# Kernel tuning notes

Hardware: AMD Instinct MI355X
Metric: run time of the kernel (lower is better)

## Reference

```python
import jax, jax.numpy as jnp
import numpy as np

HEAD_NUM = 16

def setup_inputs() -> dict:
    key = jax.random.key(0)
    kq, kk, kv = jax.random.split(key, 3)
    shape = (4, 2048, 1024)  # [B, N, C]
    return {
        "query_layer": jax.random.normal(kq, shape, dtype=jnp.float32),
        "key_layer": jax.random.normal(kk, shape, dtype=jnp.float32),
        "value_layer": jax.random.normal(kv, shape, dtype=jnp.float32),
    }

def _split_heads(x, h):
    B, N, C = x.shape
    return x.reshape(B, N, h, C // h).transpose(0, 2, 1, 3)  # [B,H,N,d]

def reference(query_layer, key_layer, value_layer):
    B, N, C = query_layer.shape
    h = HEAD_NUM
    d = C // h
    q = _split_heads(query_layer, h)
    k = _split_heads(key_layer, h)
    v = _split_heads(value_layer, h)
    scores = jnp.einsum('bhnd,bhmd->bhnm', q, k) / jnp.sqrt(jnp.asarray(d, q.dtype))
    probs = jax.nn.softmax(scores, axis=-1)
    ctx = jnp.einsum('bhnm,bhmd->bhnd', probs, v)
    return ctx.transpose(0, 2, 1, 3).reshape(B, N, C)
```

## Files before the change

kernel.cpp:

```cpp
#include <hip/hip_runtime.h>
#include <hip/hip_bf16.h>

#define B_   4
#define N_   2048
#define C_   1024
#define NT   32
#define QSCALE 0.18033688011112042f

typedef __attribute__((ext_vector_type(8)))  short short8;
typedef __attribute__((ext_vector_type(4)))  float f32x4;
typedef __attribute__((ext_vector_type(16))) float f32x16;
typedef __attribute__((ext_vector_type(2)))  int   int2v;

__device__ __forceinline__ unsigned short f2bf(float x) {
    union { __hip_bfloat16 h; unsigned short u; } c;
    c.h = __float2bfloat16(x);
    return c.u;
}
__device__ __forceinline__ float fast_exp2(float x) {
    float r; asm("v_exp_f32 %0, %1" : "=v"(r) : "v"(x)); return r;
}
__device__ __forceinline__ int cvtpk(float a, float b) {
    int r; asm("v_cvt_pk_bf16_f32 %0, %1, %2" : "=v"(r) : "v"(a), "v"(b)); return r;
}

__global__ __launch_bounds__(256) void prepack(
    const float* __restrict__ K, const float* __restrict__ V,
    unsigned short* __restrict__ Kt, unsigned short* __restrict__ Vt)
{
    __shared__ __align__(16) unsigned short vl[64 * 64];
    const int blk = blockIdx.x;
    const int t = blk & 31, head = blk >> 5;
    const int b = head >> 4, h = head & 15;
    const int tid = threadIdx.x;
    const int r = tid >> 2, cb = tid & 3;
    const size_t head_off = (size_t)b * N_ * C_ + (size_t)h * 64;
    const int kv0 = t * 64;

    {
        const float* src = K + head_off + (size_t)(kv0 + r) * C_ + cb * 16;
        f32x4 x0 = *(const f32x4*)(src);
        f32x4 x1 = *(const f32x4*)(src + 4);
        f32x4 x2 = *(const f32x4*)(src + 8);
        f32x4 x3 = *(const f32x4*)(src + 12);
        short8 p0, p1;
        #pragma unroll
        for (int i = 0; i < 4; ++i) {
            p0[i] = (short)f2bf(x0[i]); p0[i + 4] = (short)f2bf(x1[i]);
            p1[i] = (short)f2bf(x2[i]); p1[i + 4] = (short)f2bf(x3[i]);
        }
        unsigned short* dst = Kt + (size_t)blk * 4096 + r * 64;
        const int swz = (r & 7) << 3;
        *(short8*)&dst[(cb * 16) ^ swz]     = p0;
        *(short8*)&dst[(cb * 16 + 8) ^ swz] = p1;
    }
    {
        const float* src = V + head_off + (size_t)(kv0 + r) * C_ + cb * 16;
        f32x4 y0 = *(const f32x4*)(src);
        f32x4 y1 = *(const f32x4*)(src + 4);
        f32x4 y2 = *(const f32x4*)(src + 8);
        f32x4 y3 = *(const f32x4*)(src + 12);
        #pragma unroll
        for (int i = 0; i < 4; ++i) {
            vl[(cb * 16 + i) * 64 + r]      = f2bf(y0[i]);
            vl[(cb * 16 + 4 + i) * 64 + r]  = f2bf(y1[i]);
            vl[(cb * 16 + 8 + i) * 64 + r]  = f2bf(y2[i]);
            vl[(cb * 16 + 12 + i) * 64 + r] = f2bf(y3[i]);
        }
    }
    __syncthreads();
    {
        short8 q0 = *(const short8*)&vl[r * 64 + cb * 16];
        short8 q1 = *(const short8*)&vl[r * 64 + cb * 16 + 8];
        unsigned short* dst = Vt + (size_t)blk * 4096 + r * 64;
        const int swz = (r & 7) << 3;
        *(short8*)&dst[(cb * 16) ^ swz]     = q0;
        *(short8*)&dst[(cb * 16 + 8) ^ swz] = q1;
    }
}

__global__ __launch_bounds__(256, 4) void attn_fwd(
    const float* __restrict__ Q, const unsigned short* __restrict__ Kt,
    const unsigned short* __restrict__ Vt, float* __restrict__ O)
{
    __shared__ __align__(16) unsigned short klds[2][4096];
    __shared__ __align__(16) unsigned short vlds[2][4096];

    const int L = blockIdx.x;
    const int xcd = L & 7;
    const int j = L >> 3;
    const int head = xcd + 8 * (j >> 4);
    const int qt = j & 15;
    const int b = head >> 4, h = head & 15;

    const int tid  = threadIdx.x;
    const int wave = tid >> 6;
    const int lane = tid & 63;
    const int l31  = lane & 31;
    const int hi   = lane >> 5;
    const int sw8  = (l31 & 7) << 3;

    const unsigned short* kbase = Kt + (size_t)head * (NT * 4096);
    const unsigned short* vbase = Vt + (size_t)head * (NT * 4096);
    const float* qp = Q + (size_t)b * N_ * C_ + (size_t)h * 64;
    float*       op = O + (size_t)b * N_ * C_ + (size_t)h * 64;

    const int qrow = qt * 128 + wave * 32 + l31;
    short8 qfrag[4];
    {
        const float* qr = qp + (size_t)qrow * C_ + hi * 8;
        #pragma unroll
        for (int ks = 0; ks < 4; ++ks) {
            f32x4 x0 = *(const f32x4*)(qr + ks * 16);
            f32x4 x1 = *(const f32x4*)(qr + ks * 16 + 4);
            short8 a;
            #pragma unroll
            for (int i = 0; i < 4; ++i) {
                a[i]     = (short)f2bf(x0[i] * QSCALE);
                a[i + 4] = (short)f2bf(x1[i] * QSCALE);
            }
            qfrag[ks] = a;
        }
    }

    f32x16 o0 = {}, o1 = {};
    float m_r = -3.0e38f, l_r = 0.0f;

    auto stage = [&](int t, int buf) {
        const unsigned short* kg = kbase + (size_t)t * 4096 + wave * 512 + lane * 8;
        const unsigned short* vg = vbase + (size_t)t * 4096 + wave * 512 + lane * 8;
        __builtin_amdgcn_global_load_lds((const __attribute__((address_space(1))) void*)kg,
            (__attribute__((address_space(3))) void*)&klds[buf][wave * 512], 16, 0, 0);
        __builtin_amdgcn_global_load_lds((const __attribute__((address_space(1))) void*)(kg + 2048),
            (__attribute__((address_space(3))) void*)&klds[buf][2048 + wave * 512], 16, 0, 0);
        __builtin_amdgcn_global_load_lds((const __attribute__((address_space(1))) void*)vg,
            (__attribute__((address_space(3))) void*)&vlds[buf][wave * 512], 16, 0, 0);
        __builtin_amdgcn_global_load_lds((const __attribute__((address_space(1))) void*)(vg + 2048),
            (__attribute__((address_space(3))) void*)&vlds[buf][2048 + wave * 512], 16, 0, 0);
    };

    stage(0, 0);
    int cur = 0;

    for (int t = 0; t < NT; ++t) {
        asm volatile("s_waitcnt vmcnt(0)" ::: "memory");
        __syncthreads();
        if (t + 1 < NT) stage(t + 1, cur ^ 1);

        const unsigned short* kl = klds[cur];
        const unsigned short* vl = vlds[cur];

        f32x16 s0 = {}, s1 = {};
        __builtin_amdgcn_s_setprio(1);
        #pragma unroll
        for (int ks = 0; ks < 4; ++ks) {
            const int cofs = (ks * 16 + hi * 8) ^ sw8;
            short8 kf0 = *(const short8*)&kl[l31 * 64 + cofs];
            short8 kf1 = *(const short8*)&kl[(32 + l31) * 64 + cofs];
            s0 = __builtin_amdgcn_mfma_f32_32x32x16_bf16(kf0, qfrag[ks], s0, 0, 0, 0);
            s1 = __builtin_amdgcn_mfma_f32_32x32x16_bf16(kf1, qfrag[ks], s1, 0, 0, 0);
        }
        __builtin_amdgcn_s_setprio(0);

        float mx[16];
        #pragma unroll
        for (int r = 0; r < 16; ++r) mx[r] = fmaxf(s0[r], s1[r]);
        #pragma unroll
        for (int st = 8; st; st >>= 1) {
            #pragma unroll
            for (int r = 0; r < st; ++r) mx[r] = fmaxf(mx[r], mx[r + st]);
        }
        int2v msw = __builtin_amdgcn_permlane32_swap(__float_as_int(mx[0]), __float_as_int(mx[0]), false, false);
        const float rm = fmaxf(__int_as_float(msw[0]), __int_as_float(msw[1]));

        if (!__all(rm - m_r <= 8.0f)) {
            const float mnew = fmaxf(m_r, rm);
            const float corr = fast_exp2(m_r - mnew);
            m_r = mnew;
            l_r *= corr;
            #pragma unroll
            for (int r = 0; r < 16; ++r) { o0[r] *= corr; o1[r] *= corr; }
        }

        #pragma unroll
        for (int r = 0; r < 16; ++r) {
            s0[r] = fast_exp2(s0[r] - m_r);
            s1[r] = fast_exp2(s1[r] - m_r);
        }
        float aa[16];
        #pragma unroll
        for (int r = 0; r < 16; ++r) aa[r] = s0[r] + s1[r];
        #pragma unroll
        for (int st = 8; st; st >>= 1) {
            #pragma unroll
            for (int r = 0; r < st; ++r) aa[r] += aa[r + st];
        }
        int2v ssw = __builtin_amdgcn_permlane32_swap(__float_as_int(aa[0]), __float_as_int(aa[0]), false, false);
        l_r += __int_as_float(ssw[0]) + __int_as_float(ssw[1]);

        short8 pf[4];
        #pragma unroll
        for (int ct = 0; ct < 2; ++ct) {
            #pragma unroll
            for (int kss = 0; kss < 2; ++kss) {
                float e0, e1, e2, e3, e4, e5, e6, e7;
                if (ct == 0) {
                    e0 = s0[8*kss+0]; e1 = s0[8*kss+1]; e2 = s0[8*kss+2]; e3 = s0[8*kss+3];
                    e4 = s0[8*kss+4]; e5 = s0[8*kss+5]; e6 = s0[8*kss+6]; e7 = s0[8*kss+7];
                } else {
                    e0 = s1[8*kss+0]; e1 = s1[8*kss+1]; e2 = s1[8*kss+2]; e3 = s1[8*kss+3];
                    e4 = s1[8*kss+4]; e5 = s1[8*kss+5]; e6 = s1[8*kss+6]; e7 = s1[8*kss+7];
                }
                int w0 = cvtpk(e0, e1);
                int w1 = cvtpk(e2, e3);
                int w2 = cvtpk(e4, e5);
                int w3 = cvtpk(e6, e7);
                int2v sA = __builtin_amdgcn_permlane32_swap(w0, w2, false, false);
                int2v sB = __builtin_amdgcn_permlane32_swap(w1, w3, false, false);
                union { int i[4]; short8 v; } u;
                u.i[0] = sA[0]; u.i[1] = sB[0]; u.i[2] = sA[1]; u.i[3] = sB[1];
                pf[ct * 2 + kss] = u.v;
            }
        }

        __builtin_amdgcn_s_setprio(1);
        #pragma unroll
        for (int ks = 0; ks < 4; ++ks) {
            const int cofs = (ks * 16 + hi * 8) ^ sw8;
            short8 vf0 = *(const short8*)&vl[l31 * 64 + cofs];
            short8 vf1 = *(const short8*)&vl[(32 + l31) * 64 + cofs];
            o0 = __builtin_amdgcn_mfma_f32_32x32x16_bf16(vf0, pf[ks], o0, 0, 0, 0);
            o1 = __builtin_amdgcn_mfma_f32_32x32x16_bf16(vf1, pf[ks], o1, 0, 0, 0);
        }
        __builtin_amdgcn_s_setprio(0);

        cur ^= 1;
    }

    const float inv = 1.0f / l_r;
    float* orow = op + (size_t)qrow * C_;
    #pragma unroll
    for (int bb = 0; bb < 4; ++bb) {
        f32x4 w0, w1;
        #pragma unroll
        for (int i = 0; i < 4; ++i) {
            w0[i] = o0[4 * bb + i] * inv;
            w1[i] = o1[4 * bb + i] * inv;
        }
        *(f32x4*)(orow + 8 * bb + 4 * hi)      = w0;
        *(f32x4*)(orow + 32 + 8 * bb + 4 * hi) = w1;
    }
}

extern "C" void kernel_launch(void* const* d_in, const int* in_sizes, int n_in,
                              void* d_out, int out_size, void* d_ws, size_t ws_size,
                              hipStream_t stream) {
    const float* q = (const float*)d_in[0];
    const float* k = (const float*)d_in[1];
    const float* v = (const float*)d_in[2];
    float* o = (float*)d_out;
    unsigned short* Kt = (unsigned short*)d_ws;
    unsigned short* Vt = Kt + (size_t)64 * NT * 4096;
    prepack<<<dim3(64 * NT), dim3(256), 0, stream>>>(k, v, Kt, Vt);
    attn_fwd<<<dim3(1024), dim3(256), 0, stream>>>(q, Kt, Vt, o);
}
```

Before: 115.0 us.

## Prepack K/V in MFMA fragment order and load fragments directly from global

The prepack kernel now writes K and V tiles in the exact per-lane MFMA fragment order, staging through swizzled LDS, and its blocks are mapped so each XCD handles particular heads. The attention kernel drops its LDS double buffer, barriers and vmcnt waits, and loads each fragment straight from global memory with contiguous 16-byte per-lane reads, relying on the L2 cache for reuse across the 16 query tiles of a head. The max and sum reductions are also restructured to use fewer serial steps. The risk is that global-load latency is no longer hidden by async staging and that L2 and bandwidth pressure rises, since each wave now fetches the K/V tiles itself instead of sharing one copy through LDS.

```diff
diff --git a/kernel.cpp b/kernel.cpp
--- a/kernel.cpp
+++ b/kernel.cpp
@@ -28,14 +28,19 @@
     const float* __restrict__ K, const float* __restrict__ V,
     unsigned short* __restrict__ Kt, unsigned short* __restrict__ Vt)
 {
-    __shared__ __align__(16) unsigned short vl[64 * 64];
-    const int blk = blockIdx.x;
-    const int t = blk & 31, head = blk >> 5;
+    __shared__ __align__(16) unsigned short kl[4096];
+    __shared__ __align__(16) unsigned short vl[4096];
+    const int L = blockIdx.x;
+    const int xcd = L & 7;
+    const int j = L >> 3;
+    const int head = xcd + 8 * (j >> 5);
+    const int t = j & 31;
     const int b = head >> 4, h = head & 15;
     const int tid = threadIdx.x;
     const int r = tid >> 2, cb = tid & 3;
     const size_t head_off = (size_t)b * N_ * C_ + (size_t)h * 64;
     const int kv0 = t * 64;
+    const int blk_out = head * NT + t;
 
     {
         const float* src = K + head_off + (size_t)(kv0 + r) * C_ + cb * 16;
@@ -49,10 +54,9 @@
             p0[i] = (short)f2bf(x0[i]); p0[i + 4] = (short)f2bf(x1[i]);
             p1[i] = (short)f2bf(x2[i]); p1[i + 4] = (short)f2bf(x3[i]);
         }
-        unsigned short* dst = Kt + (size_t)blk * 4096 + r * 64;
         const int swz = (r & 7) << 3;
-        *(short8*)&dst[(cb * 16) ^ swz]     = p0;
-        *(short8*)&dst[(cb * 16 + 8) ^ swz] = p1;
+        *(short8*)&kl[r * 64 + ((cb * 16) ^ swz)]     = p0;
+        *(short8*)&kl[r * 64 + ((cb * 16 + 8) ^ swz)] = p1;
     }
     {
         const float* src = V + head_off + (size_t)(kv0 + r) * C_ + cb * 16;
@@ -62,20 +66,29 @@
         f32x4 y3 = *(const f32x4*)(src + 12);
         #pragma unroll
         for (int i = 0; i < 4; ++i) {
-            vl[(cb * 16 + i) * 64 + r]      = f2bf(y0[i]);
-            vl[(cb * 16 + 4 + i) * 64 + r]  = f2bf(y1[i]);
-            vl[(cb * 16 + 8 + i) * 64 + r]  = f2bf(y2[i]);
-            vl[(cb * 16 + 12 + i) * 64 + r] = f2bf(y3[i]);
+            int d0 = cb * 16 + i;
+            vl[d0 * 64 + (r ^ ((d0 & 7) << 3))] = f2bf(y0[i]);
+            int d1 = cb * 16 + 4 + i;
+            vl[d1 * 64 + (r ^ ((d1 & 7) << 3))] = f2bf(y1[i]);
+            int d2 = cb * 16 + 8 + i;
+            vl[d2 * 64 + (r ^ ((d2 & 7) << 3))] = f2bf(y2[i]);
+            int d3 = cb * 16 + 12 + i;
+            vl[d3 * 64 + (r ^ ((d3 & 7) << 3))] = f2bf(y3[i]);
         }
     }
     __syncthreads();
-    {
-        short8 q0 = *(const short8*)&vl[r * 64 + cb * 16];
-        short8 q1 = *(const short8*)&vl[r * 64 + cb * 16 + 8];
-        unsigned short* dst = Vt + (size_t)blk * 4096 + r * 64;
-        const int swz = (r & 7) << 3;
-        *(short8*)&dst[(cb * 16) ^ swz]     = q0;
-        *(short8*)&dst[(cb * 16 + 8) ^ swz] = q1;
+    #pragma unroll
+    for (int cc = 0; cc < 2; ++cc) {
+        const int c  = tid + cc * 256;
+        const int f  = c >> 6;
+        const int ln = c & 63;
+        const int row = (f & 1) * 32 + (ln & 31);
+        const int col = (f >> 1) * 16 + (ln >> 5) * 8;
+        const int sw  = (row & 7) << 3;
+        short8 kk = *(const short8*)&kl[row * 64 + (col ^ sw)];
+        short8 vv = *(const short8*)&vl[row * 64 + (col ^ sw)];
+        *(short8*)&Kt[(size_t)blk_out * 4096 + c * 8] = kk;
+        *(short8*)&Vt[(size_t)blk_out * 4096 + c * 8] = vv;
     }
 }
 
@@ -83,9 +96,6 @@
     const float* __restrict__ Q, const unsigned short* __restrict__ Kt,
     const unsigned short* __restrict__ Vt, float* __restrict__ O)
 {
-    __shared__ __align__(16) unsigned short klds[2][4096];
-    __shared__ __align__(16) unsigned short vlds[2][4096];
-
     const int L = blockIdx.x;
     const int xcd = L & 7;
     const int j = L >> 3;
@@ -98,7 +108,6 @@
     const int lane = tid & 63;
     const int l31  = lane & 31;
     const int hi   = lane >> 5;
-    const int sw8  = (l31 & 7) << 3;
 
     const unsigned short* kbase = Kt + (size_t)head * (NT * 4096);
     const unsigned short* vbase = Vt + (size_t)head * (NT * 4096);
@@ -126,47 +135,28 @@
     f32x16 o0 = {}, o1 = {};
     float m_r = -3.0e38f, l_r = 0.0f;
 
-    auto stage = [&](int t, int buf) {
-        const unsigned short* kg = kbase + (size_t)t * 4096 + wave * 512 + lane * 8;
-        const unsigned short* vg = vbase + (size_t)t * 4096 + wave * 512 + lane * 8;
-        __builtin_amdgcn_global_load_lds((const __attribute__((address_space(1))) void*)kg,
-            (__attribute__((address_space(3))) void*)&klds[buf][wave * 512], 16, 0, 0);
-        __builtin_amdgcn_global_load_lds((const __attribute__((address_space(1))) void*)(kg + 2048),
-            (__attribute__((address_space(3))) void*)&klds[buf][2048 + wave * 512], 16, 0, 0);
-        __builtin_amdgcn_global_load_lds((const __attribute__((address_space(1))) void*)vg,
-            (__attribute__((address_space(3))) void*)&vlds[buf][wave * 512], 16, 0, 0);
-        __builtin_amdgcn_global_load_lds((const __attribute__((address_space(1))) void*)(vg + 2048),
-            (__attribute__((address_space(3))) void*)&vlds[buf][2048 + wave * 512], 16, 0, 0);
-    };
-
-    stage(0, 0);
-    int cur = 0;
+    const int lofs = lane * 8;
 
     for (int t = 0; t < NT; ++t) {
-        asm volatile("s_waitcnt vmcnt(0)" ::: "memory");
-        __syncthreads();
-        if (t + 1 < NT) stage(t + 1, cur ^ 1);
-
-        const unsigned short* kl = klds[cur];
-        const unsigned short* vl = vlds[cur];
+        const unsigned short* ktp = kbase + (size_t)t * 4096;
+        const unsigned short* vtp = vbase + (size_t)t * 4096;
 
         f32x16 s0 = {}, s1 = {};
         __builtin_amdgcn_s_setprio(1);
         #pragma unroll
         for (int ks = 0; ks < 4; ++ks) {
-            const int cofs = (ks * 16 + hi * 8) ^ sw8;
-            short8 kf0 = *(const short8*)&kl[l31 * 64 + cofs];
-            short8 kf1 = *(const short8*)&kl[(32 + l31) * 64 + cofs];
+            short8 kf0 = *(const short8*)(ktp + ks * 1024 + lofs);
+            short8 kf1 = *(const short8*)(ktp + ks * 1024 + 512 + lofs);
             s0 = __builtin_amdgcn_mfma_f32_32x32x16_bf16(kf0, qfrag[ks], s0, 0, 0, 0);
             s1 = __builtin_amdgcn_mfma_f32_32x32x16_bf16(kf1, qfrag[ks], s1, 0, 0, 0);
         }
         __builtin_amdgcn_s_setprio(0);
 
-        float mx[16];
-        #pragma unroll
-        for (int r = 0; r < 16; ++r) mx[r] = fmaxf(s0[r], s1[r]);
-        #pragma unroll
-        for (int st = 8; st; st >>= 1) {
+        float mx[8];
+        #pragma unroll
+        for (int r = 0; r < 8; ++r) mx[r] = fmaxf(fmaxf(s0[r], s0[r + 8]), fmaxf(s1[r], s1[r + 8]));
+        #pragma unroll
+        for (int st = 4; st; st >>= 1) {
             #pragma unroll
             for (int r = 0; r < st; ++r) mx[r] = fmaxf(mx[r], mx[r + st]);
         }
@@ -187,11 +177,11 @@
             s0[r] = fast_exp2(s0[r] - m_r);
             s1[r] = fast_exp2(s1[r] - m_r);
         }
-        float aa[16];
-        #pragma unroll
-        for (int r = 0; r < 16; ++r) aa[r] = s0[r] + s1[r];
-        #pragma unroll
-        for (int st = 8; st; st >>= 1) {
+        float aa[8];
+        #pragma unroll
+        for (int r = 0; r < 8; ++r) aa[r] = (s0[r] + s0[r + 8]) + (s1[r] + s1[r + 8]);
+        #pragma unroll
+        for (int st = 4; st; st >>= 1) {
             #pragma unroll
             for (int r = 0; r < st; ++r) aa[r] += aa[r + st];
         }
@@ -226,15 +216,12 @@
         __builtin_amdgcn_s_setprio(1);
         #pragma unroll
         for (int ks = 0; ks < 4; ++ks) {
-            const int cofs = (ks * 16 + hi * 8) ^ sw8;
-            short8 vf0 = *(const short8*)&vl[l31 * 64 + cofs];
-            short8 vf1 = *(const short8*)&vl[(32 + l31) * 64 + cofs];
+            short8 vf0 = *(const short8*)(vtp + ks * 1024 + lofs);
+            short8 vf1 = *(const short8*)(vtp + ks * 1024 + 512 + lofs);
             o0 = __builtin_amdgcn_mfma_f32_32x32x16_bf16(vf0, pf[ks], o0, 0, 0, 0);
             o1 = __builtin_amdgcn_mfma_f32_32x32x16_bf16(vf1, pf[ks], o1, 0, 0, 0);
         }
         __builtin_amdgcn_s_setprio(0);
-
-        cur ^= 1;
     }
 
     const float inv = 1.0f / l_r;
```

After: 120.9 us. 1.05x slower.
